# Performance work log

Measured on AMD Instinct MI355X. Metric: run time of the kernel, lower is better.

The kernel has to match this reference:

```python
import jax, jax.numpy as jnp
import numpy as np

B, T, F_IN, H, OUT = 64, 2048, 128, 256, 10
K, STRIDE, C = 5, 2, 64
TC = (T - K) // STRIDE + 1  # 1022


def setup_inputs() -> dict:
    key = jax.random.key(0)
    ks = jax.random.split(key, 10)
    u = lambda k, shape, bound: jax.random.uniform(k, shape, jnp.float32, -bound, bound)
    cb = 1.0 / np.sqrt(F_IN * K)   # torch Conv1d init bound
    lb = 1.0 / np.sqrt(H)          # torch LSTMCell / Linear init bound
    return {
        "input": jax.random.normal(ks[0], (B, T, F_IN), jnp.float32),
        "r": jnp.zeros((TC, B, C), jnp.float32),
        "conv_w": u(ks[1], (C, F_IN, K), cb),
        "conv_b": u(ks[2], (C,), cb),
        "w_ih": u(ks[3], (4 * H, C), lb),
        "w_hh": u(ks[4], (4 * H, H), lb),
        "b_ih": u(ks[5], (4 * H,), lb),
        "b_hh": u(ks[6], (4 * H,), lb),
        "lin_w": u(ks[7], (OUT, H), lb),
        "lin_b": u(ks[8], (OUT,), lb),
        "batch_size": B,
    }


def reference(input, r, conv_w, conv_b, w_ih, w_hh, b_ih, b_hh, lin_w, lin_b, batch_size):
    # F.normalize default: L2 over dim=1 (the time axis here), eps=1e-12
    norm = jnp.sqrt(jnp.sum(input * input, axis=1, keepdims=True))
    x = input / jnp.maximum(norm, 1e-12)
    # Conv1d over time: [B,T,F] -> [B,F,T] -> [B,64,Tc]
    x = jnp.transpose(x, (0, 2, 1))
    y = jax.lax.conv_general_dilated(
        x, conv_w, window_strides=(STRIDE,), padding='VALID',
        dimension_numbers=('NCH', 'OIH', 'NCH')) + conv_b[None, :, None]
    lstm_in = jax.nn.relu(jnp.transpose(y, (2, 0, 1)))  # [Tc, B, 64]

    hdim = w_hh.shape[1]
    bsz = lstm_in.shape[1]

    def step(carry, xt):
        h, c = carry
        gates = xt @ w_ih.T + h @ w_hh.T + b_ih + b_hh
        i, f, g, o = jnp.split(gates, 4, axis=-1)  # torch gate order i,f,g,o
        c = jax.nn.sigmoid(f) * c + jax.nn.sigmoid(i) * jnp.tanh(g)
        h = jax.nn.sigmoid(o) * jnp.tanh(c)
        return (h, c), None

    init = (jnp.zeros((bsz, hdim), lstm_in.dtype), jnp.zeros((bsz, hdim), lstm_in.dtype))
    (h_t, _), _ = jax.lax.scan(step, init, lstm_in)
    return h_t @ lin_w.T + lin_b
```

## Files before the change

### kernel.cpp

```cpp
#include <hip/hip_runtime.h>
#include <stdint.h>

#define B_ 64
#define T_ 2048
#define F_ 128
#define H_ 256
#define TC_ 1022

typedef __bf16 bf16x8 __attribute__((ext_vector_type(8)));
typedef float f32x4 __attribute__((ext_vector_type(4)));
typedef unsigned long long u64;

__device__ __forceinline__ ushort f2bf(float f) {
    uint32_t u = __builtin_bit_cast(uint32_t, f);
    u += 0x7FFFu + ((u >> 16) & 1u);
    return (ushort)(u >> 16);
}
__device__ __forceinline__ float sigmoidf_(float x) { return 1.f / (1.f + __expf(-x)); }
__device__ __forceinline__ float tanhf_(float x) {
    x = fminf(15.f, fmaxf(-15.f, x));
    float e = __expf(2.f * x);
    return (e - 1.f) / (e + 1.f);
}

__global__ __launch_bounds__(128) void k_sqsum(const float* __restrict__ in,
                                               float* __restrict__ sq) {
    int b = blockIdx.x >> 4, tq = blockIdx.x & 15, f = threadIdx.x;
    const float* p = in + ((size_t)b * T_ + (size_t)tq * 128) * F_ + f;
    float acc = 0.f;
#pragma unroll 8
    for (int t = 0; t < 128; ++t) { float v = p[(size_t)t * F_]; acc += v * v; }
    atomicAdd(&sq[b * F_ + f], acc);
}

__global__ __launch_bounds__(256) void k_prep(const float* __restrict__ wih, const float* __restrict__ whh,
                                              const float* __restrict__ bih, const float* __restrict__ bhh,
                                              ushort* __restrict__ wbf, float* __restrict__ bias) {
    int e = blockIdx.x * 256 + threadIdx.x;
    if (e < 64 * 16 * 320) {
        int g = e / 5120, m = (e / 320) & 15, k = e % 320;
        int j = (m & 3) * 256 + g * 4 + (m >> 2);
        float v = (k < 64) ? wih[j * 64 + k] : whh[j * 256 + (k - 64)];
        wbf[e] = f2bf(v);
    }
    if (e < 1024) bias[e] = bih[e] + bhh[e];
}

__global__ __launch_bounds__(256) void k_conv(const float* __restrict__ in, const float* __restrict__ cw,
                                              const float* __restrict__ cb, const float* __restrict__ sq,
                                              ushort* __restrict__ li) {
    __shared__ float rn[128];
    __shared__ __align__(16) float xs[67 * 129];
    __shared__ __align__(16) float wl[80 * 68];
    int b = blockIdx.x >> 5, tile = blockIdx.x & 31;
    int tc0 = tile * 32;
    int tid = threadIdx.x;
    if (tid < 128) { float ss = sq[b * 128 + tid]; rn[tid] = 1.f / fmaxf(sqrtf(ss), 1e-12f); }
    __syncthreads();
    const float* ip = in + ((size_t)b * T_ + (size_t)(2 * tc0)) * F_;
    for (int i = tid; i < 67 * 128; i += 256) {
        int r = i >> 7, f = i & 127;
        int t = 2 * tc0 + r;
        xs[r * 129 + f] = (t < T_) ? ip[(size_t)r * F_ + f] * rn[f] : 0.f;
    }
    int cg = tid & 15, tcg = tid >> 4;
    float a00 = 0, a01 = 0, a10 = 0, a11 = 0, a20 = 0, a21 = 0, a30 = 0, a31 = 0;
    for (int fc = 0; fc < 8; ++fc) {
        __syncthreads();
        for (int i = tid; i < 64 * 80; i += 256) {
            int c = i / 80, j = i - c * 80;
            wl[j * 68 + c] = cw[c * 640 + fc * 80 + j];
        }
        __syncthreads();
#pragma unroll
        for (int fi = 0; fi < 16; ++fi) {
#pragma unroll
            for (int k = 0; k < 5; ++k) {
                const float4 w4 = *(const float4*)&wl[(fi * 5 + k) * 68 + cg * 4];
                float x0 = xs[(4 * tcg + k) * 129 + fc * 16 + fi];
                float x1 = xs[(4 * tcg + 2 + k) * 129 + fc * 16 + fi];
                a00 += w4.x * x0; a01 += w4.x * x1;
                a10 += w4.y * x0; a11 += w4.y * x1;
                a20 += w4.z * x0; a21 += w4.z * x1;
                a30 += w4.w * x0; a31 += w4.w * x1;
            }
        }
    }
    float bc0 = cb[cg * 4 + 0], bc1 = cb[cg * 4 + 1], bc2 = cb[cg * 4 + 2], bc3 = cb[cg * 4 + 3];
#pragma unroll
    for (int tt = 0; tt < 2; ++tt) {
        int tc = tc0 + tcg * 2 + tt;
        if (tc < TC_) {
            float v0 = fmaxf((tt ? a01 : a00) + bc0, 0.f);
            float v1 = fmaxf((tt ? a11 : a10) + bc1, 0.f);
            float v2 = fmaxf((tt ? a21 : a20) + bc2, 0.f);
            float v3 = fmaxf((tt ? a31 : a30) + bc3, 0.f);
            uint2 pk;
            pk.x = (uint32_t)f2bf(v0) | ((uint32_t)f2bf(v1) << 16);
            pk.y = (uint32_t)f2bf(v2) | ((uint32_t)f2bf(v3) << 16);
            *reinterpret_cast<uint2*>(&li[((size_t)tc * 64 + b) * 72 + cg * 4]) = pk;
        }
    }
}

__global__ __launch_bounds__(512) void k_scan(const ushort* __restrict__ li,
                                              const ushort* __restrict__ wbf,
                                              const float* __restrict__ bias,
                                              u64* __restrict__ hbuf,
                                              float* __restrict__ hfin) {
    __shared__ __align__(16) ushort Hs[16 * 264];
    int p = blockIdx.x >> 2, q = blockIdx.x & 3;
    int tid = threadIdx.x;
    int lane = tid & 63, wave = tid >> 6, l16 = lane & 15, quad = lane >> 4;
    int bb = p * 16 + l16;
    int g2a = q * 16 + 2 * wave, g2b = g2a + 1;
    int u0 = g2a * 4 + quad, u1 = g2b * 4 + quad;
    bf16x8 af0[10], af1[10];
    const ushort* wp0 = wbf + ((size_t)(g2a * 16 + l16)) * 320 + quad * 8;
    const ushort* wp1 = wbf + ((size_t)(g2b * 16 + l16)) * 320 + quad * 8;
#pragma unroll
    for (int s = 0; s < 10; ++s) { af0[s] = *(const bf16x8*)(wp0 + s * 32);
                                   af1[s] = *(const bf16x8*)(wp1 + s * 32); }
    float bi0 = bias[u0], bf0 = bias[256 + u0], bg0 = bias[512 + u0], bo0 = bias[768 + u0];
    float bi1 = bias[u1], bf1 = bias[256 + u1], bg1 = bias[512 + u1], bo1 = bias[768 + u1];
    float cs0 = 0.f, cs1 = 0.f;
    const ushort* xpp = li + ((size_t)0 * 64 + bb) * 72 + quad * 8;
    bf16x8 x0 = *(const bf16x8*)xpp;
    bf16x8 x1 = *(const bf16x8*)(xpp + 32);
#pragma unroll 1
    for (int t = 0; t < TC_; ++t) {
        f32x4 A0 = {0.f, 0.f, 0.f, 0.f}, A1 = {0.f, 0.f, 0.f, 0.f};
        A0 = __builtin_amdgcn_mfma_f32_16x16x32_bf16(af0[0], x0, A0, 0, 0, 0);
        A1 = __builtin_amdgcn_mfma_f32_16x16x32_bf16(af1[0], x0, A1, 0, 0, 0);
        A0 = __builtin_amdgcn_mfma_f32_16x16x32_bf16(af0[1], x1, A0, 0, 0, 0);
        A1 = __builtin_amdgcn_mfma_f32_16x16x32_bf16(af1[1], x1, A1, 0, 0, 0);
        if (t > 0) {
            uint tg = (uint)(t - 1);
            const u64* src = hbuf + ((size_t)((t - 1) & 1) << 13) + p * 2048 + tid * 4;
            u64 vv[4];
            bool ok;
            int guard = 0;
            do {
#pragma unroll
                for (int k = 0; k < 4; ++k)
                    vv[k] = __hip_atomic_load(src + k, __ATOMIC_RELAXED, __HIP_MEMORY_SCOPE_AGENT);
                uint m = 0;
#pragma unroll
                for (int k = 0; k < 4; ++k)
                    m |= (((uint)(vv[k] >> 16) & 0xFFFFu) ^ tg) | (((uint)(vv[k] >> 48)) ^ tg);
                ok = (m == 0);
            } while (!__all(ok) && ++guard < (1 << 14));
            {
                int b = tid >> 5, c0 = (tid * 4) & 127;
                uint4 w;
                w.x = ((uint)vv[0] & 0xFFFFu) | (((uint)(vv[0] >> 32) & 0xFFFFu) << 16);
                w.y = ((uint)vv[1] & 0xFFFFu) | (((uint)(vv[1] >> 32) & 0xFFFFu) << 16);
                w.z = ((uint)vv[2] & 0xFFFFu) | (((uint)(vv[2] >> 32) & 0xFFFFu) << 16);
                w.w = ((uint)vv[3] & 0xFFFFu) | (((uint)(vv[3] >> 32) & 0xFFFFu) << 16);
                *(uint4*)((char*)Hs + b * 528 + c0 * 4) = w;
            }
            __syncthreads();
#pragma unroll
            for (int s = 0; s < 8; ++s) {
                bf16x8 bh = *(const bf16x8*)((const char*)Hs + l16 * 528 + s * 64 + quad * 16);
                A0 = __builtin_amdgcn_mfma_f32_16x16x32_bf16(af0[2 + s], bh, A0, 0, 0, 0);
                A1 = __builtin_amdgcn_mfma_f32_16x16x32_bf16(af1[2 + s], bh, A1, 0, 0, 0);
            }
            __syncthreads();
        }
        float hv0, hv1;
        {
            float gi = A0[0] + bi0, gf = A0[1] + bf0, gg = A0[2] + bg0, go = A0[3] + bo0;
            float ii = sigmoidf_(gi), ff = sigmoidf_(gf), g2 = tanhf_(gg), oo = sigmoidf_(go);
            cs0 = ff * cs0 + ii * g2;
            hv0 = oo * tanhf_(cs0);
        }
        {
            float gi = A1[0] + bi1, gf = A1[1] + bf1, gg = A1[2] + bg1, go = A1[3] + bo1;
            float ii = sigmoidf_(gi), ff = sigmoidf_(gf), g2 = tanhf_(gg), oo = sigmoidf_(go);
            cs1 = ff * cs1 + ii * g2;
            hv1 = oo * tanhf_(cs1);
        }
        if (t == TC_ - 1) {
            hfin[u0 * 64 + bb] = hv0;
            hfin[u1 * 64 + bb] = hv1;
        } else {
            ushort h0 = f2bf(hv0), h1 = f2bf(hv1);
            uint pr0 = ((uint)h0 & 0xFFFFu) | ((uint)__shfl((int)h0, (lane + 16) & 63) << 16);
            uint pr1 = ((uint)h1 & 0xFFFFu) | ((uint)__shfl((int)h1, (lane + 16) & 63) << 16);
            if ((quad & 1) == 0) {
                uint tg2 = ((uint)t) << 16;
                u64 w0 = (u64)((pr0 & 0xFFFFu) | tg2) | ((u64)((pr0 >> 16) | tg2) << 32);
                u64 w1 = (u64)((pr1 & 0xFFFFu) | tg2) | ((u64)((pr1 >> 16) | tg2) << 32);
                int pc = 32 * q + 4 * wave + (quad >> 1);
                u64* dst = hbuf + ((size_t)(t & 1) << 13) + p * 2048 + l16 * 128;
                __hip_atomic_store(dst + pc, w0, __ATOMIC_RELAXED, __HIP_MEMORY_SCOPE_AGENT);
                __hip_atomic_store(dst + pc + 2, w1, __ATOMIC_RELAXED, __HIP_MEMORY_SCOPE_AGENT);
            }
        }
        int tn = (t + 1 < TC_) ? t + 1 : t;
        const ushort* xpn = li + ((size_t)tn * 64 + bb) * 72 + quad * 8;
        x0 = *(const bf16x8*)xpn;
        x1 = *(const bf16x8*)(xpn + 32);
    }
}

__global__ __launch_bounds__(64) void k_fin(const float* __restrict__ hfin, const float* __restrict__ lw,
                                            const float* __restrict__ lb, float* __restrict__ out) {
    int o = blockIdx.x, b = threadIdx.x;
    float acc = lb[o];
    const float* wp = lw + o * 256;
#pragma unroll 4
    for (int u2 = 0; u2 < 256; ++u2) acc += hfin[u2 * 64 + b] * wp[u2];
    out[b * 10 + o] = acc;
}

extern "C" void kernel_launch(void* const* d_in, const int* in_sizes, int n_in,
                              void* d_out, int out_size, void* d_ws, size_t ws_size,
                              hipStream_t stream) {
    const float* in  = (const float*)d_in[0];
    const float* cw  = (const float*)d_in[2];
    const float* cb  = (const float*)d_in[3];
    const float* wih = (const float*)d_in[4];
    const float* whh = (const float*)d_in[5];
    const float* bih = (const float*)d_in[6];
    const float* bhh = (const float*)d_in[7];
    const float* lw  = (const float*)d_in[8];
    const float* lb  = (const float*)d_in[9];
    float* out = (float*)d_out;

    char* ws = (char*)d_ws;
    float*  sq   = (float*)(ws + 0);
    u64*    hbuf = (u64*)(ws + 32768);
    float*  bias = (float*)(ws + 163840);
    float*  hfin = (float*)(ws + 167936);
    ushort* wbf  = (ushort*)(ws + 233472);
    ushort* li   = (ushort*)(ws + 888832);

    hipMemsetAsync(sq, 0, 32768, stream);
    hipMemsetAsync(hbuf, 0xFF, 131072, stream);

    k_sqsum<<<1024, 128, 0, stream>>>(in, sq);
    k_prep<<<1280, 256, 0, stream>>>(wih, whh, bih, bhh, wbf, bias);
    k_conv<<<2048, 256, 0, stream>>>(in, cw, cb, sq, li);
    k_scan<<<16, 512, 0, stream>>>(li, wbf, bias, hbuf, hfin);
    k_fin<<<10, 64, 0, stream>>>(hfin, lw, lb, out);
}
```

Baseline: 2.795 ms.

## Repartition LSTM scan into 8 gate-slices per 32-batch group, interleaving two batch halves

```diff
diff --git a/kernel.cpp b/kernel.cpp
--- a/kernel.cpp
+++ b/kernel.cpp
@@ -103,17 +103,16 @@
     }
 }
 
-__global__ __launch_bounds__(512) void k_scan(const ushort* __restrict__ li,
+__global__ __launch_bounds__(256) void k_scan(const ushort* __restrict__ li,
                                               const ushort* __restrict__ wbf,
                                               const float* __restrict__ bias,
                                               u64* __restrict__ hbuf,
                                               float* __restrict__ hfin) {
     __shared__ __align__(16) ushort Hs[16 * 264];
-    int p = blockIdx.x >> 2, q = blockIdx.x & 3;
+    int p = blockIdx.x >> 3, bq = blockIdx.x & 7;
     int tid = threadIdx.x;
     int lane = tid & 63, wave = tid >> 6, l16 = lane & 15, quad = lane >> 4;
-    int bb = p * 16 + l16;
-    int g2a = q * 16 + 2 * wave, g2b = g2a + 1;
+    int g2a = bq * 8 + 2 * wave, g2b = g2a + 1;
     int u0 = g2a * 4 + quad, u1 = g2b * 4 + quad;
     bf16x8 af0[10], af1[10];
     const ushort* wp0 = wbf + ((size_t)(g2a * 16 + l16)) * 320 + quad * 8;
@@ -123,85 +122,105 @@
                                    af1[s] = *(const bf16x8*)(wp1 + s * 32); }
     float bi0 = bias[u0], bf0 = bias[256 + u0], bg0 = bias[512 + u0], bo0 = bias[768 + u0];
     float bi1 = bias[u1], bf1 = bias[256 + u1], bg1 = bias[512 + u1], bo1 = bias[768 + u1];
-    float cs0 = 0.f, cs1 = 0.f;
-    const ushort* xpp = li + ((size_t)0 * 64 + bb) * 72 + quad * 8;
-    bf16x8 x0 = *(const bf16x8*)xpp;
-    bf16x8 x1 = *(const bf16x8*)(xpp + 32);
+    float cs[2][2] = {{0.f, 0.f}, {0.f, 0.f}};
+    bf16x8 xl0[2], xl1[2];
+#pragma unroll
+    for (int g = 0; g < 2; ++g) {
+        const ushort* xpp = li + ((size_t)(32 * p + 16 * g + l16)) * 72 + quad * 8;
+        xl0[g] = *(const bf16x8*)xpp;
+        xl1[g] = *(const bf16x8*)(xpp + 32);
+    }
 #pragma unroll 1
     for (int t = 0; t < TC_; ++t) {
-        f32x4 A0 = {0.f, 0.f, 0.f, 0.f}, A1 = {0.f, 0.f, 0.f, 0.f};
-        A0 = __builtin_amdgcn_mfma_f32_16x16x32_bf16(af0[0], x0, A0, 0, 0, 0);
-        A1 = __builtin_amdgcn_mfma_f32_16x16x32_bf16(af1[0], x0, A1, 0, 0, 0);
-        A0 = __builtin_amdgcn_mfma_f32_16x16x32_bf16(af0[1], x1, A0, 0, 0, 0);
-        A1 = __builtin_amdgcn_mfma_f32_16x16x32_bf16(af1[1], x1, A1, 0, 0, 0);
-        if (t > 0) {
-            uint tg = (uint)(t - 1);
-            const u64* src = hbuf + ((size_t)((t - 1) & 1) << 13) + p * 2048 + tid * 4;
-            u64 vv[4];
-            bool ok;
-            int guard = 0;
-            do {
-#pragma unroll
-                for (int k = 0; k < 4; ++k)
+#pragma unroll
+        for (int g = 0; g < 2; ++g) {
+            const u64* src = hbuf + ((((size_t)((t - 1) & 1)) * 4 + p * 2 + g) << 11) + tid * 8;
+            u64 vv[8];
+            if (t > 0) {
+#pragma unroll
+                for (int k = 0; k < 8; ++k)
                     vv[k] = __hip_atomic_load(src + k, __ATOMIC_RELAXED, __HIP_MEMORY_SCOPE_AGENT);
+            }
+            f32x4 A0 = {0.f, 0.f, 0.f, 0.f}, A1 = {0.f, 0.f, 0.f, 0.f};
+            A0 = __builtin_amdgcn_mfma_f32_16x16x32_bf16(af0[0], xl0[g], A0, 0, 0, 0);
+            A1 = __builtin_amdgcn_mfma_f32_16x16x32_bf16(af1[0], xl0[g], A1, 0, 0, 0);
+            A0 = __builtin_amdgcn_mfma_f32_16x16x32_bf16(af0[1], xl1[g], A0, 0, 0, 0);
+            A1 = __builtin_amdgcn_mfma_f32_16x16x32_bf16(af1[1], xl1[g], A1, 0, 0, 0);
+            if (t > 0) {
+                uint tg = (uint)(t - 1);
                 uint m = 0;
 #pragma unroll
-                for (int k = 0; k < 4; ++k)
+                for (int k = 0; k < 8; ++k)
                     m |= (((uint)(vv[k] >> 16) & 0xFFFFu) ^ tg) | (((uint)(vv[k] >> 48)) ^ tg);
-                ok = (m == 0);
-            } while (!__all(ok) && ++guard < (1 << 14));
+                bool ok = (m == 0);
+                int guard = 0;
+                while (!__all(ok) && ++guard < (1 << 14)) {
+#pragma unroll
+                    for (int k = 0; k < 8; ++k)
+                        vv[k] = __hip_atomic_load(src + k, __ATOMIC_RELAXED, __HIP_MEMORY_SCOPE_AGENT);
+                    m = 0;
+#pragma unroll
+                    for (int k = 0; k < 8; ++k)
+                        m |= (((uint)(vv[k] >> 16) & 0xFFFFu) ^ tg) | (((uint)(vv[k] >> 48)) ^ tg);
+                    ok = (m == 0);
+                }
+                {
+                    int b = tid >> 4, c0 = (tid & 15) * 8;
+                    uint w[8];
+#pragma unroll
+                    for (int k = 0; k < 8; ++k)
+                        w[k] = ((uint)vv[k] & 0xFFFFu) | (((uint)(vv[k] >> 32) & 0xFFFFu) << 16);
+                    uint4 wa, wb;
+                    wa.x = w[0]; wa.y = w[1]; wa.z = w[2]; wa.w = w[3];
+                    wb.x = w[4]; wb.y = w[5]; wb.z = w[6]; wb.w = w[7];
+                    *(uint4*)((char*)Hs + b * 528 + c0 * 4) = wa;
+                    *(uint4*)((char*)Hs + b * 528 + c0 * 4 + 16) = wb;
+                }
+                __syncthreads();
+#pragma unroll
+                for (int s = 0; s < 8; ++s) {
+                    bf16x8 bh = *(const bf16x8*)((const char*)Hs + l16 * 528 + s * 64 + quad * 16);
+                    A0 = __builtin_amdgcn_mfma_f32_16x16x32_bf16(af0[2 + s], bh, A0, 0, 0, 0);
+                    A1 = __builtin_amdgcn_mfma_f32_16x16x32_bf16(af1[2 + s], bh, A1, 0, 0, 0);
+                }
+                __syncthreads();
+            }
+            int bb = 32 * p + 16 * g + l16;
+            float hv0, hv1;
             {
-                int b = tid >> 5, c0 = (tid * 4) & 127;
-                uint4 w;
-                w.x = ((uint)vv[0] & 0xFFFFu) | (((uint)(vv[0] >> 32) & 0xFFFFu) << 16);
-                w.y = ((uint)vv[1] & 0xFFFFu) | (((uint)(vv[1] >> 32) & 0xFFFFu) << 16);
-                w.z = ((uint)vv[2] & 0xFFFFu) | (((uint)(vv[2] >> 32) & 0xFFFFu) << 16);
-                w.w = ((uint)vv[3] & 0xFFFFu) | (((uint)(vv[3] >> 32) & 0xFFFFu) << 16);
-                *(uint4*)((char*)Hs + b * 528 + c0 * 4) = w;
-            }
-            __syncthreads();
-#pragma unroll
-            for (int s = 0; s < 8; ++s) {
-                bf16x8 bh = *(const bf16x8*)((const char*)Hs + l16 * 528 + s * 64 + quad * 16);
-                A0 = __builtin_amdgcn_mfma_f32_16x16x32_bf16(af0[2 + s], bh, A0, 0, 0, 0);
-                A1 = __builtin_amdgcn_mfma_f32_16x16x32_bf16(af1[2 + s], bh, A1, 0, 0, 0);
-            }
-            __syncthreads();
-        }
-        float hv0, hv1;
-        {
-            float gi = A0[0] + bi0, gf = A0[1] + bf0, gg = A0[2] + bg0, go = A0[3] + bo0;
-            float ii = sigmoidf_(gi), ff = sigmoidf_(gf), g2 = tanhf_(gg), oo = sigmoidf_(go);
-            cs0 = ff * cs0 + ii * g2;
-            hv0 = oo * tanhf_(cs0);
-        }
-        {
-            float gi = A1[0] + bi1, gf = A1[1] + bf1, gg = A1[2] + bg1, go = A1[3] + bo1;
-            float ii = sigmoidf_(gi), ff = sigmoidf_(gf), g2 = tanhf_(gg), oo = sigmoidf_(go);
-            cs1 = ff * cs1 + ii * g2;
-            hv1 = oo * tanhf_(cs1);
-        }
-        if (t == TC_ - 1) {
-            hfin[u0 * 64 + bb] = hv0;
-            hfin[u1 * 64 + bb] = hv1;
-        } else {
-            ushort h0 = f2bf(hv0), h1 = f2bf(hv1);
-            uint pr0 = ((uint)h0 & 0xFFFFu) | ((uint)__shfl((int)h0, (lane + 16) & 63) << 16);
-            uint pr1 = ((uint)h1 & 0xFFFFu) | ((uint)__shfl((int)h1, (lane + 16) & 63) << 16);
-            if ((quad & 1) == 0) {
-                uint tg2 = ((uint)t) << 16;
-                u64 w0 = (u64)((pr0 & 0xFFFFu) | tg2) | ((u64)((pr0 >> 16) | tg2) << 32);
-                u64 w1 = (u64)((pr1 & 0xFFFFu) | tg2) | ((u64)((pr1 >> 16) | tg2) << 32);
-                int pc = 32 * q + 4 * wave + (quad >> 1);
-                u64* dst = hbuf + ((size_t)(t & 1) << 13) + p * 2048 + l16 * 128;
-                __hip_atomic_store(dst + pc, w0, __ATOMIC_RELAXED, __HIP_MEMORY_SCOPE_AGENT);
-                __hip_atomic_store(dst + pc + 2, w1, __ATOMIC_RELAXED, __HIP_MEMORY_SCOPE_AGENT);
-            }
-        }
-        int tn = (t + 1 < TC_) ? t + 1 : t;
-        const ushort* xpn = li + ((size_t)tn * 64 + bb) * 72 + quad * 8;
-        x0 = *(const bf16x8*)xpn;
-        x1 = *(const bf16x8*)(xpn + 32);
+                float gi = A0[0] + bi0, gf = A0[1] + bf0, gg = A0[2] + bg0, go = A0[3] + bo0;
+                float ii = sigmoidf_(gi), ff = sigmoidf_(gf), g2 = tanhf_(gg), oo = sigmoidf_(go);
+                cs[g][0] = ff * cs[g][0] + ii * g2;
+                hv0 = oo * tanhf_(cs[g][0]);
+            }
+            {
+                float gi = A1[0] + bi1, gf = A1[1] + bf1, gg = A1[2] + bg1, go = A1[3] + bo1;
+                float ii = sigmoidf_(gi), ff = sigmoidf_(gf), g2 = tanhf_(gg), oo = sigmoidf_(go);
+                cs[g][1] = ff * cs[g][1] + ii * g2;
+                hv1 = oo * tanhf_(cs[g][1]);
+            }
+            if (t == TC_ - 1) {
+                hfin[u0 * 64 + bb] = hv0;
+                hfin[u1 * 64 + bb] = hv1;
+            } else {
+                ushort h0 = f2bf(hv0), h1 = f2bf(hv1);
+                uint pr0 = ((uint)h0 & 0xFFFFu) | ((uint)__shfl((int)h0, (lane + 16) & 63) << 16);
+                uint pr1 = ((uint)h1 & 0xFFFFu) | ((uint)__shfl((int)h1, (lane + 16) & 63) << 16);
+                if ((quad & 1) == 0) {
+                    uint tg2 = ((uint)t) << 16;
+                    u64 w0 = (u64)((pr0 & 0xFFFFu) | tg2) | ((u64)((pr0 >> 16) | tg2) << 32);
+                    u64 w1 = (u64)((pr1 & 0xFFFFu) | tg2) | ((u64)((pr1 >> 16) | tg2) << 32);
+                    int pc = 16 * bq + 4 * wave + (quad >> 1);
+                    u64* dst = hbuf + ((((size_t)(t & 1)) * 4 + p * 2 + g) << 11) + l16 * 128;
+                    __hip_atomic_store(dst + pc, w0, __ATOMIC_RELAXED, __HIP_MEMORY_SCOPE_AGENT);
+                    __hip_atomic_store(dst + pc + 2, w1, __ATOMIC_RELAXED, __HIP_MEMORY_SCOPE_AGENT);
+                }
+            }
+            int tn = (t + 1 < TC_) ? t + 1 : t;
+            const ushort* xpn = li + ((size_t)tn * 64 + bb) * 72 + quad * 8;
+            xl0[g] = *(const bf16x8*)xpn;
+            xl1[g] = *(const bf16x8*)(xpn + 32);
+        }
     }
 }
 
@@ -243,6 +262,6 @@
     k_sqsum<<<1024, 128, 0, stream>>>(in, sq);
     k_prep<<<1280, 256, 0, stream>>>(wih, whh, bih, bhh, wbf, bias);
     k_conv<<<2048, 256, 0, stream>>>(in, cw, cb, sq, li);
-    k_scan<<<16, 512, 0, stream>>>(li, wbf, bias, hbuf, hfin);
+    k_scan<<<16, 256, 0, stream>>>(li, wbf, bias, hbuf, hfin);
     k_fin<<<10, 64, 0, stream>>>(hfin, lw, lb, out);
 }
```

Measured after the change: 5.213 ms. +86.5%, slower.

## Replace tagged-payload polling with per-block flag handshake and bf16 h image

Applied to the files above, without the earlier changes.

```diff
diff --git a/kernel.cpp b/kernel.cpp
--- a/kernel.cpp
+++ b/kernel.cpp
@@ -9,6 +9,7 @@
 
 typedef __bf16 bf16x8 __attribute__((ext_vector_type(8)));
 typedef float f32x4 __attribute__((ext_vector_type(4)));
+typedef uint u32x4 __attribute__((ext_vector_type(4)));
 typedef unsigned long long u64;
 
 __device__ __forceinline__ ushort f2bf(float f) {
@@ -16,11 +17,13 @@
     u += 0x7FFFu + ((u >> 16) & 1u);
     return (ushort)(u >> 16);
 }
-__device__ __forceinline__ float sigmoidf_(float x) { return 1.f / (1.f + __expf(-x)); }
+__device__ __forceinline__ float sigmoidf_(float x) {
+    return __builtin_amdgcn_rcpf(1.f + __expf(-x));
+}
 __device__ __forceinline__ float tanhf_(float x) {
     x = fminf(15.f, fmaxf(-15.f, x));
     float e = __expf(2.f * x);
-    return (e - 1.f) / (e + 1.f);
+    return 1.f - 2.f * __builtin_amdgcn_rcpf(e + 1.f);
 }
 
 __global__ __launch_bounds__(128) void k_sqsum(const float* __restrict__ in,
@@ -109,9 +112,12 @@
                                               u64* __restrict__ hbuf,
                                               float* __restrict__ hfin) {
     __shared__ __align__(16) ushort Hs[16 * 264];
+    uint* flags = (uint*)hbuf;
+    ushort* himg = (ushort*)((char*)hbuf + 4096);
     int p = blockIdx.x >> 2, q = blockIdx.x & 3;
     int tid = threadIdx.x;
-    int lane = tid & 63, wave = tid >> 6, l16 = lane & 15, quad = lane >> 4;
+    int lane = tid & 63, l16 = lane & 15, quad = lane >> 4;
+    int wave = tid >> 6;
     int bb = p * 16 + l16;
     int g2a = q * 16 + 2 * wave, g2b = g2a + 1;
     int u0 = g2a * 4 + quad, u1 = g2b * 4 + quad;
@@ -129,6 +135,10 @@
     bf16x8 x1 = *(const bf16x8*)(xpp + 32);
 #pragma unroll 1
     for (int t = 0; t < TC_; ++t) {
+        int tn = (t + 1 < TC_) ? t + 1 : t;
+        const ushort* xpn = li + ((size_t)tn * 64 + bb) * 72 + quad * 8;
+        bf16x8 nx0 = *(const bf16x8*)xpn;
+        bf16x8 nx1 = *(const bf16x8*)(xpn + 32);
         f32x4 A0 = {0.f, 0.f, 0.f, 0.f}, A1 = {0.f, 0.f, 0.f, 0.f};
         A0 = __builtin_amdgcn_mfma_f32_16x16x32_bf16(af0[0], x0, A0, 0, 0, 0);
         A1 = __builtin_amdgcn_mfma_f32_16x16x32_bf16(af1[0], x0, A1, 0, 0, 0);
@@ -136,29 +146,24 @@
         A1 = __builtin_amdgcn_mfma_f32_16x16x32_bf16(af1[1], x1, A1, 0, 0, 0);
         if (t > 0) {
             uint tg = (uint)(t - 1);
-            const u64* src = hbuf + ((size_t)((t - 1) & 1) << 13) + p * 2048 + tid * 4;
-            u64 vv[4];
+            const uint* fp = flags + ((size_t)((t - 1) & 1)) * 16 + p * 4;
+            u32x4 fv;
             bool ok;
             int guard = 0;
             do {
-#pragma unroll
-                for (int k = 0; k < 4; ++k)
-                    vv[k] = __hip_atomic_load(src + k, __ATOMIC_RELAXED, __HIP_MEMORY_SCOPE_AGENT);
-                uint m = 0;
-#pragma unroll
-                for (int k = 0; k < 4; ++k)
-                    m |= (((uint)(vv[k] >> 16) & 0xFFFFu) ^ tg) | (((uint)(vv[k] >> 48)) ^ tg);
-                ok = (m == 0);
+                asm volatile(
+                    "global_load_dwordx4 %0, %1, off sc0 sc1\n\t"
+                    "s_waitcnt vmcnt(0)"
+                    : "=&v"(fv) : "v"(fp) : "memory");
+                ok = (fv.x == tg) && (fv.y == tg) && (fv.z == tg) && (fv.w == tg);
             } while (!__all(ok) && ++guard < (1 << 14));
-            {
-                int b = tid >> 5, c0 = (tid * 4) & 127;
-                uint4 w;
-                w.x = ((uint)vv[0] & 0xFFFFu) | (((uint)(vv[0] >> 32) & 0xFFFFu) << 16);
-                w.y = ((uint)vv[1] & 0xFFFFu) | (((uint)(vv[1] >> 32) & 0xFFFFu) << 16);
-                w.z = ((uint)vv[2] & 0xFFFFu) | (((uint)(vv[2] >> 32) & 0xFFFFu) << 16);
-                w.w = ((uint)vv[3] & 0xFFFFu) | (((uint)(vv[3] >> 32) & 0xFFFFu) << 16);
-                *(uint4*)((char*)Hs + b * 528 + c0 * 4) = w;
-            }
+            const ushort* dimg = himg + (((size_t)((t - 1) & 1) * 4 + p) << 12) + tid * 8;
+            u32x4 dv;
+            asm volatile(
+                "global_load_dwordx4 %0, %1, off sc0 sc1\n\t"
+                "s_waitcnt vmcnt(0)"
+                : "=&v"(dv) : "v"(dimg) : "memory");
+            *(u32x4*)((char*)Hs + (tid >> 5) * 528 + (tid & 31) * 16) = dv;
             __syncthreads();
 #pragma unroll
             for (int s = 0; s < 8; ++s) {
@@ -166,7 +171,6 @@
                 A0 = __builtin_amdgcn_mfma_f32_16x16x32_bf16(af0[2 + s], bh, A0, 0, 0, 0);
                 A1 = __builtin_amdgcn_mfma_f32_16x16x32_bf16(af1[2 + s], bh, A1, 0, 0, 0);
             }
-            __syncthreads();
         }
         float hv0, hv1;
         {
@@ -186,22 +190,27 @@
             hfin[u1 * 64 + bb] = hv1;
         } else {
             ushort h0 = f2bf(hv0), h1 = f2bf(hv1);
-            uint pr0 = ((uint)h0 & 0xFFFFu) | ((uint)__shfl((int)h0, (lane + 16) & 63) << 16);
-            uint pr1 = ((uint)h1 & 0xFFFFu) | ((uint)__shfl((int)h1, (lane + 16) & 63) << 16);
+            uint pr0 = ((uint)h0) | ((uint)__shfl((int)h0, (lane + 16) & 63) << 16);
+            uint pr1 = ((uint)h1) | ((uint)__shfl((int)h1, (lane + 16) & 63) << 16);
             if ((quad & 1) == 0) {
-                uint tg2 = ((uint)t) << 16;
-                u64 w0 = (u64)((pr0 & 0xFFFFu) | tg2) | ((u64)((pr0 >> 16) | tg2) << 32);
-                u64 w1 = (u64)((pr1 & 0xFFFFu) | tg2) | ((u64)((pr1 >> 16) | tg2) << 32);
-                int pc = 32 * q + 4 * wave + (quad >> 1);
-                u64* dst = hbuf + ((size_t)(t & 1) << 13) + p * 2048 + l16 * 128;
-                __hip_atomic_store(dst + pc, w0, __ATOMIC_RELAXED, __HIP_MEMORY_SCOPE_AGENT);
-                __hip_atomic_store(dst + pc + 2, w1, __ATOMIC_RELAXED, __HIP_MEMORY_SCOPE_AGENT);
+                ushort* dst = himg + (((size_t)(t & 1) * 4 + p) << 12) + l16 * 256;
+                asm volatile(
+                    "global_store_dword %0, %2, off sc0 sc1\n\t"
+                    "global_store_dword %1, %3, off sc0 sc1\n\t"
+                    "s_waitcnt vmcnt(0)"
+                    :: "v"(dst + u0), "v"(dst + u1), "v"(pr0), "v"(pr1)
+                    : "memory");
             }
         }
-        int tn = (t + 1 < TC_) ? t + 1 : t;
-        const ushort* xpn = li + ((size_t)tn * 64 + bb) * 72 + quad * 8;
-        x0 = *(const bf16x8*)xpn;
-        x1 = *(const bf16x8*)(xpn + 32);
+        __syncthreads();
+        if (tid == 0 && t < TC_ - 1) {
+            uint* fdst = flags + ((size_t)(t & 1)) * 16 + p * 4 + q;
+            uint tv = (uint)t;
+            asm volatile(
+                "global_store_dword %0, %1, off sc0 sc1"
+                :: "v"(fdst), "v"(tv) : "memory");
+        }
+        x0 = nx0; x1 = nx1;
     }
 }
 
@@ -238,7 +247,7 @@
     ushort* li   = (ushort*)(ws + 888832);
 
     hipMemsetAsync(sq, 0, 32768, stream);
-    hipMemsetAsync(hbuf, 0xFF, 131072, stream);
+    hipMemsetAsync(hbuf, 0xFF, 69632 + 4096, stream);
 
     k_sqsum<<<1024, 128, 0, stream>>>(in, sq);
     k_prep<<<1280, 256, 0, stream>>>(wih, whh, bih, bhh, wbf, bias);
```

Result: slower. 2.996 ms (+7.2%).
